# Performance work log

Hardware: AMD Instinct MI355X
Metric: run time of the kernel (lower is better)

## Reference

```python
import jax, jax.numpy as jnp
import numpy as np

B, T, C = 1, 2048, 2048
H, KV, D = 16, 4, 128
PAST = 2048


def setup_inputs() -> dict:
    key = jax.random.key(0)
    ks = jax.random.split(key, 11)
    return {
        "x": jax.random.normal(ks[0], (B, T, C), jnp.float32),
        "ve": jax.random.normal(ks[1], (B, T, KV * D), jnp.float32),
        "cos": jax.random.normal(ks[2], (1, T, 1, D // 2), jnp.float32),
        "sin": jax.random.normal(ks[3], (1, T, 1, D // 2), jnp.float32),
        "past_key": jax.random.normal(ks[4], (B, PAST, KV, D), jnp.float32),
        "past_value": jax.random.normal(ks[5], (B, PAST, KV, D), jnp.float32),
        "Wq": jax.random.normal(ks[6], (C, H * D), jnp.float32) * 0.02,
        "Wk": jax.random.normal(ks[7], (C, KV * D), jnp.float32) * 0.02,
        "Wv": jax.random.normal(ks[8], (C, KV * D), jnp.float32) * 0.02,
        "Wo": jax.random.normal(ks[9], (H * D, C), jnp.float32) * 0.02,
        "Wg": jax.random.normal(ks[10], (12, KV), jnp.float32),
    }


def _rmsnorm(x):
    return x * jax.lax.rsqrt(jnp.mean(x * x, axis=-1, keepdims=True) + 1e-6)


def _rope(x, cos, sin):
    # x: (B,T,heads,D); cos/sin: (1,T,1,D//2) broadcast over heads
    d = x.shape[-1] // 2
    x1, x2 = x[..., :d], x[..., d:]
    return jnp.concatenate([x1 * cos + x2 * sin, -x1 * sin + x2 * cos], axis=-1)


def reference(x, ve, cos, sin, past_key, past_value, Wq, Wk, Wv, Wo, Wg):
    Bx, Tx, Cx = x.shape
    G = H // KV
    q = (x @ Wq).reshape(Bx, Tx, H, D)
    k = (x @ Wk).reshape(Bx, Tx, KV, D)
    v = (x @ Wv).reshape(Bx, Tx, KV, D)
    # value-embedding gate: 3*sigmoid over first 12 channels of x
    gate = 3.0 * jax.nn.sigmoid(x[..., :12] @ Wg)  # (B,T,KV)
    v = v + gate[..., None] * ve.reshape(Bx, Tx, KV, D)
    q = _rmsnorm(_rope(q, cos, sin)) * 1.2
    k = _rmsnorm(_rope(k, cos, sin)) * 1.2
    present_key = jnp.concatenate([past_key, k], axis=1)    # (B,S,KV,D)
    present_value = jnp.concatenate([past_value, v], axis=1)
    S = present_key.shape[1]
    q_t = q.transpose(0, 2, 1, 3)                           # (B,H,T,D)
    k_t = present_key.transpose(0, 2, 1, 3)                 # (B,KV,S,D)
    v_t = present_value.transpose(0, 2, 1, 3)
    # GQA expansion: repeat each kv head G times -> (B,H,S,D)
    k_t = jnp.broadcast_to(k_t[:, :, None], (Bx, KV, G, S, D)).reshape(Bx, H, S, D)
    v_t = jnp.broadcast_to(v_t[:, :, None], (Bx, KV, G, S, D)).reshape(Bx, H, S, D)
    scale = D ** -0.5
    scores = jnp.einsum("bhtd,bhsd->bhts", q_t, k_t) * scale
    query_pos = jnp.arange(S - Tx, S)[:, None]
    key_pos = jnp.arange(S)[None, :]
    causal = key_pos <= query_pos                           # (T,S)
    scores = jnp.where(causal[None, None], scores, -jnp.inf)
    w = jax.nn.softmax(scores, axis=-1)
    y = jnp.einsum("bhts,bhsd->bthd", w, v_t).reshape(Bx, Tx, H * D)
    y = y @ Wo
    return (y, present_key, present_value)
```

## Files before the change

kernel.cpp:

```cpp
#include <hip/hip_runtime.h>
#include <hip/hip_bf16.h>
#include <math.h>

typedef __attribute__((ext_vector_type(8))) short short8;
typedef __attribute__((ext_vector_type(4))) short short4v;
typedef __attribute__((ext_vector_type(4))) float f32x4;

#define DEV __device__ __forceinline__

DEV short f2bf(float f) {
  unsigned u = __builtin_bit_cast(unsigned, f);
  unsigned r = (u + 0x7FFFu + ((u >> 16) & 1u)) >> 16;
  return (short)r;
}

DEV float bf2f(short s) {
  unsigned u = ((unsigned)(unsigned short)s) << 16;
  return __builtin_bit_cast(float, u);
}

DEV short f2h(float f) {
  _Float16 h = (_Float16)f;
  return __builtin_bit_cast(short, h);
}

DEV float h2f(short s) {
  return (float)__builtin_bit_cast(_Float16, s);
}

DEV unsigned cvt_pk_bf16(float lo, float hi) {
  unsigned r;
  asm("v_cvt_pk_bf16_f32 %0, %1, %2" : "=v"(r) : "v"(lo), "v"(hi));
  return r;
}

DEV void gload_lds16(const void* g, void* l) {
  __builtin_amdgcn_global_load_lds((const __attribute__((address_space(1))) void*)g,
                                   (__attribute__((address_space(3))) void*)l, 16, 0, 0);
}

__global__ __launch_bounds__(256) void gemm_m64_f32(const short* __restrict__ A,
                                                    const short* __restrict__ BT,
                                                    float* __restrict__ C,
                                                    int M, int N, int K) {
  __shared__ __attribute__((aligned(16))) short As[2][64 * 64];
  __shared__ __attribute__((aligned(16))) short Bs[2][128 * 64];
  const int tid = threadIdx.x;
  const int w = tid >> 6, l = tid & 63;
  const int g = l >> 4, lr = l & 15;
  int nbx = gridDim.x, nwg = nbx * gridDim.y;
  int flat = blockIdx.y * nbx + blockIdx.x;
  int qq = nwg >> 3;
  int f2 = (flat & 7) * qq + (flat >> 3);
  const int m0 = (f2 / nbx) * 64, n0 = (f2 % nbx) * 128;
  const int wr = w >> 1, wc = w & 1;
  f32x4 acc[2][4] = {};

  auto stage = [&](int buf, int k0) {
#pragma unroll
    for (int it = 0; it < 2; ++it) {
      int idx = it * 256 + tid;
      int row = idx >> 3;
      int scol = ((idx & 7) * 16) ^ ((row & 7) << 4);
      gload_lds16(A + (size_t)(m0 + row) * K + k0 + (scol >> 1), As[buf] + idx * 8);
    }
#pragma unroll
    for (int it = 0; it < 4; ++it) {
      int idx = it * 256 + tid;
      int row = idx >> 3;
      int scol = ((idx & 7) * 16) ^ ((row & 7) << 4);
      gload_lds16(BT + (size_t)(n0 + row) * K + k0 + (scol >> 1), Bs[buf] + idx * 8);
    }
  };

  stage(0, 0);
  __syncthreads();
  int cur = 0;
  for (int k0 = 0; k0 < K; k0 += 64) {
    if (k0 + 64 < K) stage(cur ^ 1, k0 + 64);
#pragma unroll
    for (int ki = 0; ki < 2; ++ki) {
      const int kcol = (ki * 64 + g * 16) ^ ((lr & 7) << 4);
      short8 af[2], bfr[4];
#pragma unroll
      for (int i = 0; i < 2; ++i)
        af[i] = *(const short8*)(As[cur] + (((wr * 32 + i * 16 + lr) * 128 + kcol) >> 1));
#pragma unroll
      for (int i = 0; i < 4; ++i)
        bfr[i] = *(const short8*)(Bs[cur] + (((wc * 64 + i * 16 + lr) * 128 + kcol) >> 1));
#pragma unroll
      for (int mi = 0; mi < 2; ++mi)
#pragma unroll
        for (int ni = 0; ni < 4; ++ni)
          acc[mi][ni] = __builtin_amdgcn_mfma_f32_16x16x32_bf16(af[mi], bfr[ni], acc[mi][ni], 0, 0, 0);
    }
    __syncthreads();
    cur ^= 1;
  }
#pragma unroll
  for (int mi = 0; mi < 2; ++mi)
#pragma unroll
    for (int ni = 0; ni < 4; ++ni) {
      int row = m0 + wr * 32 + mi * 16 + g * 4;
      int col = n0 + wc * 64 + ni * 16 + lr;
#pragma unroll
      for (int r = 0; r < 4; ++r)
        C[(size_t)(row + r) * N + col] = acc[mi][ni][r];
    }
}

__global__ __launch_bounds__(256) void gemm_m64_bf16(const short* __restrict__ A,
                                                     const short* __restrict__ BT,
                                                     short* __restrict__ C,
                                                     int M, int N, int K) {
  __shared__ __attribute__((aligned(16))) short As[2][64 * 64];
  __shared__ __attribute__((aligned(16))) short Bs[2][128 * 64];
  const int tid = threadIdx.x;
  const int w = tid >> 6, l = tid & 63;
  const int g = l >> 4, lr = l & 15;
  int nbx = gridDim.x, nwg = nbx * gridDim.y;
  int flat = blockIdx.y * nbx + blockIdx.x;
  int qq = nwg >> 3;
  int f2 = (flat & 7) * qq + (flat >> 3);
  const int m0 = (f2 / nbx) * 64, n0 = (f2 % nbx) * 128;
  const int wr = w >> 1, wc = w & 1;
  f32x4 acc[2][4] = {};

  auto stage = [&](int buf, int k0) {
#pragma unroll
    for (int it = 0; it < 2; ++it) {
      int idx = it * 256 + tid;
      int row = idx >> 3;
      int scol = ((idx & 7) * 16) ^ ((row & 7) << 4);
      gload_lds16(A + (size_t)(m0 + row) * K + k0 + (scol >> 1), As[buf] + idx * 8);
    }
#pragma unroll
    for (int it = 0; it < 4; ++it) {
      int idx = it * 256 + tid;
      int row = idx >> 3;
      int scol = ((idx & 7) * 16) ^ ((row & 7) << 4);
      gload_lds16(BT + (size_t)(n0 + row) * K + k0 + (scol >> 1), Bs[buf] + idx * 8);
    }
  };

  stage(0, 0);
  __syncthreads();
  int cur = 0;
  for (int k0 = 0; k0 < K; k0 += 64) {
    if (k0 + 64 < K) stage(cur ^ 1, k0 + 64);
#pragma unroll
    for (int ki = 0; ki < 2; ++ki) {
      const int kcol = (ki * 64 + g * 16) ^ ((lr & 7) << 4);
      short8 af[2], bfr[4];
#pragma unroll
      for (int i = 0; i < 2; ++i)
        af[i] = *(const short8*)(As[cur] + (((wr * 32 + i * 16 + lr) * 128 + kcol) >> 1));
#pragma unroll
      for (int i = 0; i < 4; ++i)
        bfr[i] = *(const short8*)(Bs[cur] + (((wc * 64 + i * 16 + lr) * 128 + kcol) >> 1));
#pragma unroll
      for (int mi = 0; mi < 2; ++mi)
#pragma unroll
        for (int ni = 0; ni < 4; ++ni)
          acc[mi][ni] = __builtin_amdgcn_mfma_f32_16x16x32_bf16(af[mi], bfr[ni], acc[mi][ni], 0, 0, 0);
    }
    __syncthreads();
    cur ^= 1;
  }
#pragma unroll
  for (int mi = 0; mi < 2; ++mi)
#pragma unroll
    for (int ni = 0; ni < 4; ++ni) {
      int row = m0 + wr * 32 + mi * 16 + g * 4;
      int col = n0 + wc * 64 + ni * 16 + lr;
#pragma unroll
      for (int r = 0; r < 4; ++r)
        C[(size_t)(row + r) * N + col] = f2bf(acc[mi][ni][r]);
    }
}

__global__ __launch_bounds__(256) void prep(const float* __restrict__ x,
                                            short* __restrict__ xb,
                                            const float* __restrict__ Wq,
                                            const float* __restrict__ Wk,
                                            const float* __restrict__ Wv,
                                            const float* __restrict__ Wo,
                                            short* __restrict__ WTqkv,
                                            short* __restrict__ WToT) {
  __shared__ float tile[32][33];
  int bid = blockIdx.x;
  int tid = threadIdx.x;
  if (bid < 4096) {
    int i = bid * 256 + tid;
    float4 v = ((const float4*)x)[i];
    short4v o;
    o.x = f2bf(v.x); o.y = f2bf(v.y); o.z = f2bf(v.z); o.w = f2bf(v.w);
    ((short4v*)xb)[i] = o;
    return;
  }
  int b = bid - 4096;
  int bx = b % 160, by = b / 160;
  const float* W;
  short* WT;
  int N, cb;
  if (bx < 64) { W = Wq; WT = WTqkv; N = 2048; cb = bx; }
  else if (bx < 80) { W = Wk; WT = WTqkv + (size_t)2048 * 2048; N = 512; cb = bx - 64; }
  else if (bx < 96) { W = Wv; WT = WTqkv + (size_t)2560 * 2048; N = 512; cb = bx - 80; }
  else { W = Wo; WT = WToT; N = 2048; cb = bx - 96; }
  int tx = tid & 31, ty = tid >> 5;
  int c0 = cb * 32, r0 = by * 32;
#pragma unroll
  for (int i = 0; i < 4; ++i)
    tile[ty + i * 8][tx] = W[(size_t)(r0 + ty + i * 8) * N + c0 + tx];
  __syncthreads();
#pragma unroll
  for (int i = 0; i < 4; ++i)
    WT[(size_t)(c0 + ty + i * 8) * 2048 + r0 + tx] = f2bf(tile[tx][ty + i * 8]);
}

__global__ __launch_bounds__(256) void qkv_post(const short* __restrict__ qkv,
                                                const float* __restrict__ cosb,
                                                const float* __restrict__ sinb,
                                                const float* __restrict__ x,
                                                const float* __restrict__ ve,
                                                const float* __restrict__ Wg,
                                                float* __restrict__ outPK,
                                                float* __restrict__ outPV,
                                                short* __restrict__ qb,
                                                short* __restrict__ kb) {
  int gw = (blockIdx.x * 256 + threadIdx.x) >> 6;
  int l = threadIdx.x & 63;
  int t = gw / 24, u = gw - t * 24;
  if (t >= 2048) return;
  if (u < 20) {
    float c = cosb[t * 64 + l], s = sinb[t * 64 + l];
    const short* src = qkv + (size_t)t * 3072 + (u < 16 ? u * 128 : 2048 + (u - 16) * 128);
    float x1 = bf2f(src[l]), x2 = bf2f(src[64 + l]);
    float lo = x1 * c + x2 * s;
    float hi = x2 * c - x1 * s;
    float ss = lo * lo + hi * hi;
#pragma unroll
    for (int d = 1; d < 64; d <<= 1) ss += __shfl_xor(ss, d, 64);
    float r = rsqrtf(ss * (1.0f / 128.0f) + 1e-6f) * 1.2f;
    if (u < 16) {
      const float SCQ = 0.08838834764831845f * 1.4426950408889634f;
      float rq = r * SCQ;
      size_t b = ((size_t)u * 2048 + t) * 128;
      qb[b + l] = f2bf(lo * rq);
      qb[b + 64 + l] = f2bf(hi * rq);
    } else {
      lo *= r; hi *= r;
      int kvh = u - 16;
      size_t b = ((size_t)(2048 + t) * 4 + kvh) * 128;
      outPK[b + l] = lo;
      outPK[b + 64 + l] = hi;
      size_t b2 = ((size_t)kvh * 4096 + 2048 + t) * 128;
      kb[b2 + l] = f2bf(lo);
      kb[b2 + 64 + l] = f2bf(hi);
    }
  } else {
    int kv = u - 20;
    float z = 0.f;
#pragma unroll
    for (int j = 0; j < 12; ++j) z += x[(size_t)t * 2048 + j] * Wg[j * 4 + kv];
    float gate = 3.0f / (1.0f + expf(-z));
    const short* vr = qkv + (size_t)t * 3072 + 2560 + kv * 128;
    const float* vei = ve + (size_t)t * 512 + kv * 128;
    float v0 = bf2f(vr[l]) + gate * vei[l];
    float v1 = bf2f(vr[64 + l]) + gate * vei[64 + l];
    size_t b = ((size_t)(2048 + t) * 4 + kv) * 128;
    outPV[b + l] = v0;
    outPV[b + 64 + l] = v1;
  }
}

__global__ __launch_bounds__(256) void past_copy(const float* __restrict__ pk,
                                                 float* __restrict__ outPK,
                                                 short* __restrict__ kb) {
  int i = blockIdx.x * 256 + threadIdx.x;
  int d = i & 127, kv = (i >> 7) & 3, s = i >> 9;
  float a = pk[i];
  outPK[i] = a;
  kb[((size_t)kv * 4096 + s) * 128 + d] = f2bf(a);
}

__global__ __launch_bounds__(256) void v_transpose(const float* __restrict__ pv,
                                                   float* __restrict__ outPV,
                                                   short* __restrict__ vbT) {
  __shared__ float tile[32][33];
  int tx = threadIdx.x & 31, ty = threadIdx.x >> 5;
  int c0 = blockIdx.x * 32, r0 = blockIdx.y * 32;
  if (r0 < 2048) {
#pragma unroll
    for (int i = 0; i < 4; ++i) {
      float v = pv[(size_t)(r0 + ty + i * 8) * 512 + c0 + tx];
      tile[ty + i * 8][tx] = v;
      outPV[(size_t)(r0 + ty + i * 8) * 512 + c0 + tx] = v;
    }
  } else {
#pragma unroll
    for (int i = 0; i < 4; ++i)
      tile[ty + i * 8][tx] = outPV[(size_t)(r0 + ty + i * 8) * 512 + c0 + tx];
  }
  __syncthreads();
#pragma unroll
  for (int i = 0; i < 4; ++i)
    vbT[(size_t)(c0 + ty + i * 8) * 4096 + r0 + tx] = f2bf(tile[tx][ty + i * 8]);
}

__global__ __launch_bounds__(256, 2) void attn(const short* __restrict__ qb,
                                               const short* __restrict__ kb,
                                               const short* __restrict__ vbT,
                                               short* __restrict__ Po,
                                               float* __restrict__ ml) {
  extern __shared__ __attribute__((aligned(16))) short smem[];
  short* Ks = smem;
  short* Vs = smem + 16384;
  const int tid = threadIdx.x, w = tid >> 6, l = tid & 63;
  const int g = l >> 4, lr = l & 15;
  const int lid = blockIdx.x;
  const int qbi = 15 - (lid >> 5);
  const int sub = lid & 31;
  const int h = sub >> 1, cls = sub & 1;
  const int kv = h >> 2;
  const int qw = qbi * 128 + w * 32;
  char* Pw = (char*)(smem + 32768) + w * 2048;
  const short* gK = kb + (size_t)kv * 4096 * 128;
  const short* gV = vbT + (size_t)kv * 128 * 4096;
  const int nT = 34 + 2 * qbi;
  const int cnt = (nT - cls + 1) >> 1;

  short8 aq[2][4];
#pragma unroll
  for (int u = 0; u < 2; ++u)
#pragma unroll
    for (int c4 = 0; c4 < 4; ++c4)
      aq[u][c4] = *(const short8*)(qb + ((size_t)(h * 2048 + qw + u * 16 + lr)) * 128 + c4 * 32 + g * 8);

  float m_r[2] = {-INFINITY, -INFINITY};
  float l_r[2] = {0.f, 0.f};
  f32x4 o[2][8] = {};

  const int rK = tid >> 4, cKs = ((tid & 15) * 16) ^ ((rK & 7) << 4);
  const int rV = tid >> 3, cVs = ((tid & 7) * 16) ^ ((rV & 7) << 4);
  const short* kptr = gK + (size_t)(cls * 64 + rK) * 128 + (cKs >> 1);
  const short* vptr = gV + (size_t)rV * 4096 + cls * 64 + (cVs >> 1);
  short* kdst = Ks + w * 512;
  short* vdst = Vs + w * 512;

  auto stageK = [&](int buf) {
#pragma unroll
    for (int it = 0; it < 4; ++it)
      gload_lds16(kptr + it * 2048, kdst + buf * 8192 + it * 2048);
    kptr += 16384;
  };
  auto stageV = [&](int buf) {
#pragma unroll
    for (int it = 0; it < 4; ++it)
      gload_lds16(vptr + (size_t)it * 131072, vdst + buf * 8192 + it * 2048);
    vptr += 128;
  };

  stageK(0);
  stageV(0);
  __syncthreads();
  int cur = 0;
  for (int i = 0; i < cnt; ++i) {
    const int s0 = (cls + 2 * i) * 64;
    if (i + 1 < cnt) {
      stageK(cur ^ 1);
      stageV(cur ^ 1);
    }
    f32x4 sc[2][4] = {};
    __builtin_amdgcn_s_setprio(1);
#pragma unroll
    for (int cc = 0; cc < 4; ++cc) {
      const int rb = cur * 8192 + (cc * 16 + lr) * 128;
      short8 bk[4];
#pragma unroll
      for (int c4 = 0; c4 < 4; ++c4)
        bk[c4] = *(const short8*)(Ks + rb + (((c4 * 64 + g * 16) ^ ((lr & 7) << 4)) >> 1));
#pragma unroll
      for (int c4 = 0; c4 < 4; ++c4) {
        sc[0][cc] = __builtin_amdgcn_mfma_f32_16x16x32_bf16(bk[c4], aq[0][c4], sc[0][cc], 0, 0, 0);
        sc[1][cc] = __builtin_amdgcn_mfma_f32_16x16x32_bf16(bk[c4], aq[1][c4], sc[1][cc], 0, 0, 0);
      }
    }
    __builtin_amdgcn_s_setprio(0);
    if (s0 + 63 > 2048 + qw) {
#pragma unroll
      for (int u = 0; u < 2; ++u)
#pragma unroll
        for (int cc = 0; cc < 4; ++cc)
#pragma unroll
          for (int r = 0; r < 4; ++r)
            sc[u][cc][r] = (s0 + cc * 16 + g * 4 + r <= 2048 + qw + u * 16 + lr)
                               ? sc[u][cc][r] : -INFINITY;
    }
    short8 ap[2][2];
#pragma unroll
    for (int u = 0; u < 2; ++u) {
      float pmax = -INFINITY;
#pragma unroll
      for (int cc = 0; cc < 4; ++cc) {
        float a = fmaxf(fmaxf(sc[u][cc][0], sc[u][cc][1]), fmaxf(sc[u][cc][2], sc[u][cc][3]));
        pmax = fmaxf(pmax, a);
      }
      if (!__all(pmax - m_r[u] <= 8.0f)) {
        float tm = fmaxf(pmax, __shfl_xor(pmax, 16, 64));
        tm = fmaxf(tm, __shfl_xor(tm, 32, 64));
        float mn = fmaxf(m_r[u], tm);
        float corr = exp2f(m_r[u] - mn);
        m_r[u] = mn;
        l_r[u] *= corr;
        float co[4];
#pragma unroll
        for (int r = 0; r < 4; ++r) co[r] = __shfl(corr, (l & 48) | (g * 4 + r), 64);
#pragma unroll
        for (int d8 = 0; d8 < 8; ++d8) {
          f32x4 tt = o[u][d8];
#pragma unroll
          for (int r = 0; r < 4; ++r) tt[r] *= co[r];
          o[u][d8] = tt;
        }
      }
      float ps = 0.f;
#pragma unroll
      for (int cc = 0; cc < 4; ++cc) {
        float p0 = exp2f(sc[u][cc][0] - m_r[u]);
        float p1 = exp2f(sc[u][cc][1] - m_r[u]);
        float p2 = exp2f(sc[u][cc][2] - m_r[u]);
        float p3 = exp2f(sc[u][cc][3] - m_r[u]);
        ps += (p0 + p1) + (p2 + p3);
        unsigned pk0 = cvt_pk_bf16(p0, p1);
        unsigned pk1 = cvt_pk_bf16(p2, p3);
        int off8 = (lr * 128 + cc * 32 + g * 8) ^ ((lr & 7) << 4);
        unsigned long long pq = (unsigned long long)pk0 | ((unsigned long long)pk1 << 32);
        *(unsigned long long*)(Pw + off8) = pq;
      }
      l_r[u] += ps;
#pragma unroll
      for (int ks = 0; ks < 2; ++ks)
        ap[u][ks] = *(const short8*)(Pw + ((lr * 128 + ks * 64 + g * 16) ^ ((lr & 7) << 4)));
    }
    __builtin_amdgcn_s_setprio(1);
#pragma unroll
    for (int d8 = 0; d8 < 8; ++d8) {
      const int rb = cur * 8192 + (d8 * 16 + lr) * 64;
      short8 bv0 = *(const short8*)(Vs + rb + (((0 * 64 + g * 16) ^ ((lr & 7) << 4)) >> 1));
      short8 bv1 = *(const short8*)(Vs + rb + (((1 * 64 + g * 16) ^ ((lr & 7) << 4)) >> 1));
      o[0][d8] = __builtin_amdgcn_mfma_f32_16x16x32_bf16(ap[0][0], bv0, o[0][d8], 0, 0, 0);
      o[0][d8] = __builtin_amdgcn_mfma_f32_16x16x32_bf16(ap[0][1], bv1, o[0][d8], 0, 0, 0);
      o[1][d8] = __builtin_amdgcn_mfma_f32_16x16x32_bf16(ap[1][0], bv0, o[1][d8], 0, 0, 0);
      o[1][d8] = __builtin_amdgcn_mfma_f32_16x16x32_bf16(ap[1][1], bv1, o[1][d8], 0, 0, 0);
    }
    __builtin_amdgcn_s_setprio(0);
    __syncthreads();
    cur ^= 1;
  }
#pragma unroll
  for (int u = 0; u < 2; ++u) {
    float ls = l_r[u];
    ls += __shfl_xor(ls, 16, 64);
    ls += __shfl_xor(ls, 32, 64);
    float inv = 1.0f / ls;
    float invo[4];
#pragma unroll
    for (int r = 0; r < 4; ++r) invo[r] = __shfl(inv, (l & 48) | (g * 4 + r), 64);
#pragma unroll
    for (int d8 = 0; d8 < 8; ++d8)
#pragma unroll
      for (int r = 0; r < 4; ++r)
        Po[((size_t)(cls * 16 + h) * 2048 + qw + u * 16 + g * 4 + r) * 128 + d8 * 16 + lr] =
            f2h(o[u][d8][r] * invo[r]);
    if (g == 0) {
      float2 v;
      v.x = m_r[u];
      v.y = ls;
      ((float2*)ml)[(size_t)(cls * 16 + h) * 2048 + qw + u * 16 + lr] = v;
    }
  }
}

__global__ __launch_bounds__(256) void attn_merge(const short* __restrict__ Po,
                                                  const float* __restrict__ ml,
                                                  short* __restrict__ ya) {
  int i = blockIdx.x * 256 + threadIdx.x;
  int q = i >> 8, rem = i & 255, h = rem >> 4, oct = rem & 15;
  float mc[2], lc[2];
#pragma unroll
  for (int c = 0; c < 2; ++c) {
    float2 v = ((const float2*)ml)[(size_t)(c * 16 + h) * 2048 + q];
    mc[c] = v.x; lc[c] = v.y;
  }
  float m = fmaxf(mc[0], mc[1]);
  float wsum = 0.f, acc[8] = {};
#pragma unroll
  for (int c = 0; c < 2; ++c) {
    float wc = lc[c] * exp2f(mc[c] - m);
    wsum += wc;
    short8 p = *(const short8*)(Po + ((size_t)(c * 16 + h) * 2048 + q) * 128 + oct * 8);
#pragma unroll
    for (int j = 0; j < 8; ++j) acc[j] += wc * h2f(p[j]);
  }
  float inv = 1.0f / wsum;
  short8 ov;
#pragma unroll
  for (int j = 0; j < 8; ++j) ov[j] = f2bf(acc[j] * inv);
  *(short8*)(ya + (size_t)q * 2048 + h * 128 + oct * 8) = ov;
}

extern "C" void kernel_launch(void* const* d_in, const int* in_sizes, int n_in,
                              void* d_out, int out_size, void* d_ws, size_t ws_size,
                              hipStream_t stream) {
  const float* x = (const float*)d_in[0];
  const float* ve = (const float*)d_in[1];
  const float* cosb = (const float*)d_in[2];
  const float* sinb = (const float*)d_in[3];
  const float* past_key = (const float*)d_in[4];
  const float* past_value = (const float*)d_in[5];
  const float* Wq = (const float*)d_in[6];
  const float* Wk = (const float*)d_in[7];
  const float* Wv = (const float*)d_in[8];
  const float* Wo = (const float*)d_in[9];
  const float* Wg = (const float*)d_in[10];

  float* outY = (float*)d_out;
  float* outPK = outY + 4194304;
  float* outPV = outPK + 2097152;

  short* base = (short*)d_ws;
  short* WToT = base;
  short* WTqkv = base + 4194304;
  short* xb = WTqkv + (size_t)6291456;
  short* qkv = xb + (size_t)4194304;
  short* qb = qkv + (size_t)12582912;
  short* kb = qb + (size_t)4194304;
  short* vbT = kb + (size_t)2097152;
  short* ya = vbT + (size_t)2097152;
  short* Po = WTqkv;
  float* mlb = (float*)(base + 20971520);

  static bool attr_set = false;
  if (!attr_set) {
    (void)hipFuncSetAttribute((const void*)attn,
                              hipFuncAttributeMaxDynamicSharedMemorySize, 73728);
    attr_set = true;
  }

  prep<<<14336, 256, 0, stream>>>(x, xb, Wq, Wk, Wv, Wo, WTqkv, WToT);

  gemm_m64_bf16<<<dim3(24, 32), 256, 0, stream>>>(xb, WTqkv, qkv, 2048, 3072, 2048);

  qkv_post<<<12288, 256, 0, stream>>>(qkv, cosb, sinb, x, ve, Wg, outPK, outPV, qb, kb);
  past_copy<<<4096, 256, 0, stream>>>(past_key, outPK, kb);
  v_transpose<<<dim3(16, 128), 256, 0, stream>>>(past_value, outPV, vbT);

  attn<<<512, 256, 73728, stream>>>(qb, kb, vbT, Po, mlb);
  attn_merge<<<2048, 256, 0, stream>>>(Po, mlb, ya);

  gemm_m64_f32<<<dim3(16, 32), 256, 0, stream>>>(ya, WToT, outY, 2048, 2048, 2048);
}
```

Baseline: 181.0 us.

## Fuse RoPE, RMSNorm and value gating into the QKV GEMM epilogue

The QKV projection GEMM now stages its fp32 accumulator tile in shared memory and applies RoPE, RMSNorm, the Q scaling and the value-embedding gate directly in the epilogue. This removes the separate qkv_post kernel and the bf16 round trip of the qkv intermediate through global memory. Because no bf16 rounding happens before normalization, precision improves slightly. In exchange the GEMM epilogue gets longer, and shared memory grows to 48KB to hold the 64x132 fp32 tile, which could lower occupancy.

```diff
diff --git a/kernel.cpp b/kernel.cpp
--- a/kernel.cpp
+++ b/kernel.cpp
@@ -37,6 +37,132 @@
 DEV void gload_lds16(const void* g, void* l) {
   __builtin_amdgcn_global_load_lds((const __attribute__((address_space(1))) void*)g,
                                    (__attribute__((address_space(3))) void*)l, 16, 0, 0);
+}
+
+__global__ __launch_bounds__(256) void gemm_qkv_fused(const short* __restrict__ A,
+                                                      const short* __restrict__ BT,
+                                                      const float* __restrict__ cosb,
+                                                      const float* __restrict__ sinb,
+                                                      const float* __restrict__ x,
+                                                      const float* __restrict__ ve,
+                                                      const float* __restrict__ Wg,
+                                                      float* __restrict__ outPK,
+                                                      float* __restrict__ outPV,
+                                                      short* __restrict__ qb,
+                                                      short* __restrict__ kb) {
+  const int K = 2048;
+  __shared__ __attribute__((aligned(16))) char smem[49152];
+  short* As0 = (short*)smem;
+  short* Bs0 = (short*)(smem + 16384);
+  const int tid = threadIdx.x;
+  const int w = tid >> 6, l = tid & 63;
+  const int g = l >> 4, lr = l & 15;
+  int nbx = gridDim.x, nwg = nbx * gridDim.y;
+  int flat = blockIdx.y * nbx + blockIdx.x;
+  int qq = nwg >> 3;
+  int f2 = (flat & 7) * qq + (flat >> 3);
+  const int m0 = (f2 / nbx) * 64;
+  const int j = f2 % nbx;
+  const int n0 = j * 128;
+  const int wr = w >> 1, wc = w & 1;
+  f32x4 acc[2][4] = {};
+
+  auto stage = [&](int buf, int k0) {
+#pragma unroll
+    for (int it = 0; it < 2; ++it) {
+      int idx = it * 256 + tid;
+      int row = idx >> 3;
+      int scol = ((idx & 7) * 16) ^ ((row & 7) << 4);
+      gload_lds16(A + (size_t)(m0 + row) * K + k0 + (scol >> 1), As0 + buf * 4096 + idx * 8);
+    }
+#pragma unroll
+    for (int it = 0; it < 4; ++it) {
+      int idx = it * 256 + tid;
+      int row = idx >> 3;
+      int scol = ((idx & 7) * 16) ^ ((row & 7) << 4);
+      gload_lds16(BT + (size_t)(n0 + row) * K + k0 + (scol >> 1), Bs0 + buf * 8192 + idx * 8);
+    }
+  };
+
+  stage(0, 0);
+  __syncthreads();
+  int cur = 0;
+  for (int k0 = 0; k0 < K; k0 += 64) {
+    if (k0 + 64 < K) stage(cur ^ 1, k0 + 64);
+#pragma unroll
+    for (int ki = 0; ki < 2; ++ki) {
+      const int kcol = (ki * 64 + g * 16) ^ ((lr & 7) << 4);
+      short8 af[2], bfr[4];
+#pragma unroll
+      for (int i = 0; i < 2; ++i)
+        af[i] = *(const short8*)(As0 + cur * 4096 + (((wr * 32 + i * 16 + lr) * 128 + kcol) >> 1));
+#pragma unroll
+      for (int i = 0; i < 4; ++i)
+        bfr[i] = *(const short8*)(Bs0 + cur * 8192 + (((wc * 64 + i * 16 + lr) * 128 + kcol) >> 1));
+#pragma unroll
+      for (int mi = 0; mi < 2; ++mi)
+#pragma unroll
+        for (int ni = 0; ni < 4; ++ni)
+          acc[mi][ni] = __builtin_amdgcn_mfma_f32_16x16x32_bf16(af[mi], bfr[ni], acc[mi][ni], 0, 0, 0);
+    }
+    __syncthreads();
+    cur ^= 1;
+  }
+  float* tile = (float*)smem;
+#pragma unroll
+  for (int mi = 0; mi < 2; ++mi)
+#pragma unroll
+    for (int ni = 0; ni < 4; ++ni) {
+      int rrow = wr * 32 + mi * 16 + g * 4;
+      int col = wc * 64 + ni * 16 + lr;
+#pragma unroll
+      for (int r = 0; r < 4; ++r)
+        tile[(rrow + r) * 132 + col] = acc[mi][ni][r];
+    }
+  __syncthreads();
+  const float SCQ = 0.08838834764831845f * 1.4426950408889634f;
+  for (int rr = 0; rr < 16; ++rr) {
+    int tl = w * 16 + rr;
+    int t = m0 + tl;
+    float x1 = tile[tl * 132 + l];
+    float x2 = tile[tl * 132 + 64 + l];
+    if (j < 20) {
+      float c = cosb[t * 64 + l], s = sinb[t * 64 + l];
+      float lo = x1 * c + x2 * s;
+      float hi = x2 * c - x1 * s;
+      float ss = lo * lo + hi * hi;
+#pragma unroll
+      for (int d = 1; d < 64; d <<= 1) ss += __shfl_xor(ss, d, 64);
+      float r = rsqrtf(ss * (1.0f / 128.0f) + 1e-6f) * 1.2f;
+      if (j < 16) {
+        float rq = r * SCQ;
+        size_t b = ((size_t)j * 2048 + t) * 128;
+        qb[b + l] = f2bf(lo * rq);
+        qb[b + 64 + l] = f2bf(hi * rq);
+      } else {
+        lo *= r; hi *= r;
+        int kvh = j - 16;
+        size_t b = ((size_t)(2048 + t) * 4 + kvh) * 128;
+        outPK[b + l] = lo;
+        outPK[b + 64 + l] = hi;
+        size_t b2 = ((size_t)kvh * 4096 + 2048 + t) * 128;
+        kb[b2 + l] = f2bf(lo);
+        kb[b2 + 64 + l] = f2bf(hi);
+      }
+    } else {
+      int kv = j - 20;
+      float z = 0.f;
+#pragma unroll
+      for (int jj = 0; jj < 12; ++jj) z += x[(size_t)t * 2048 + jj] * Wg[jj * 4 + kv];
+      float gate = 3.0f / (1.0f + expf(-z));
+      const float* vei = ve + (size_t)t * 512 + kv * 128;
+      float v0 = x1 + gate * vei[l];
+      float v1 = x2 + gate * vei[64 + l];
+      size_t b = ((size_t)(2048 + t) * 4 + kv) * 128;
+      outPV[b + l] = v0;
+      outPV[b + 64 + l] = v1;
+    }
+  }
 }
 
 __global__ __launch_bounds__(256) void gemm_m64_f32(const short* __restrict__ A,
@@ -106,76 +232,6 @@
 #pragma unroll
       for (int r = 0; r < 4; ++r)
         C[(size_t)(row + r) * N + col] = acc[mi][ni][r];
-    }
-}
-
-__global__ __launch_bounds__(256) void gemm_m64_bf16(const short* __restrict__ A,
-                                                     const short* __restrict__ BT,
-                                                     short* __restrict__ C,
-                                                     int M, int N, int K) {
-  __shared__ __attribute__((aligned(16))) short As[2][64 * 64];
-  __shared__ __attribute__((aligned(16))) short Bs[2][128 * 64];
-  const int tid = threadIdx.x;
-  const int w = tid >> 6, l = tid & 63;
-  const int g = l >> 4, lr = l & 15;
-  int nbx = gridDim.x, nwg = nbx * gridDim.y;
-  int flat = blockIdx.y * nbx + blockIdx.x;
-  int qq = nwg >> 3;
-  int f2 = (flat & 7) * qq + (flat >> 3);
-  const int m0 = (f2 / nbx) * 64, n0 = (f2 % nbx) * 128;
-  const int wr = w >> 1, wc = w & 1;
-  f32x4 acc[2][4] = {};
-
-  auto stage = [&](int buf, int k0) {
-#pragma unroll
-    for (int it = 0; it < 2; ++it) {
-      int idx = it * 256 + tid;
-      int row = idx >> 3;
-      int scol = ((idx & 7) * 16) ^ ((row & 7) << 4);
-      gload_lds16(A + (size_t)(m0 + row) * K + k0 + (scol >> 1), As[buf] + idx * 8);
-    }
-#pragma unroll
-    for (int it = 0; it < 4; ++it) {
-      int idx = it * 256 + tid;
-      int row = idx >> 3;
-      int scol = ((idx & 7) * 16) ^ ((row & 7) << 4);
-      gload_lds16(BT + (size_t)(n0 + row) * K + k0 + (scol >> 1), Bs[buf] + idx * 8);
-    }
-  };
-
-  stage(0, 0);
-  __syncthreads();
-  int cur = 0;
-  for (int k0 = 0; k0 < K; k0 += 64) {
-    if (k0 + 64 < K) stage(cur ^ 1, k0 + 64);
-#pragma unroll
-    for (int ki = 0; ki < 2; ++ki) {
-      const int kcol = (ki * 64 + g * 16) ^ ((lr & 7) << 4);
-      short8 af[2], bfr[4];
-#pragma unroll
-      for (int i = 0; i < 2; ++i)
-        af[i] = *(const short8*)(As[cur] + (((wr * 32 + i * 16 + lr) * 128 + kcol) >> 1));
-#pragma unroll
-      for (int i = 0; i < 4; ++i)
-        bfr[i] = *(const short8*)(Bs[cur] + (((wc * 64 + i * 16 + lr) * 128 + kcol) >> 1));
-#pragma unroll
-      for (int mi = 0; mi < 2; ++mi)
-#pragma unroll
-        for (int ni = 0; ni < 4; ++ni)
-          acc[mi][ni] = __builtin_amdgcn_mfma_f32_16x16x32_bf16(af[mi], bfr[ni], acc[mi][ni], 0, 0, 0);
-    }
-    __syncthreads();
-    cur ^= 1;
-  }
-#pragma unroll
-  for (int mi = 0; mi < 2; ++mi)
-#pragma unroll
-    for (int ni = 0; ni < 4; ++ni) {
-      int row = m0 + wr * 32 + mi * 16 + g * 4;
-      int col = n0 + wc * 64 + ni * 16 + lr;
-#pragma unroll
-      for (int r = 0; r < 4; ++r)
-        C[(size_t)(row + r) * N + col] = f2bf(acc[mi][ni][r]);
     }
 }
 
@@ -216,62 +272,6 @@
 #pragma unroll
   for (int i = 0; i < 4; ++i)
     WT[(size_t)(c0 + ty + i * 8) * 2048 + r0 + tx] = f2bf(tile[tx][ty + i * 8]);
-}
-
-__global__ __launch_bounds__(256) void qkv_post(const short* __restrict__ qkv,
-                                                const float* __restrict__ cosb,
-                                                const float* __restrict__ sinb,
-                                                const float* __restrict__ x,
-                                                const float* __restrict__ ve,
-                                                const float* __restrict__ Wg,
-                                                float* __restrict__ outPK,
-                                                float* __restrict__ outPV,
-                                                short* __restrict__ qb,
-                                                short* __restrict__ kb) {
-  int gw = (blockIdx.x * 256 + threadIdx.x) >> 6;
-  int l = threadIdx.x & 63;
-  int t = gw / 24, u = gw - t * 24;
-  if (t >= 2048) return;
-  if (u < 20) {
-    float c = cosb[t * 64 + l], s = sinb[t * 64 + l];
-    const short* src = qkv + (size_t)t * 3072 + (u < 16 ? u * 128 : 2048 + (u - 16) * 128);
-    float x1 = bf2f(src[l]), x2 = bf2f(src[64 + l]);
-    float lo = x1 * c + x2 * s;
-    float hi = x2 * c - x1 * s;
-    float ss = lo * lo + hi * hi;
-#pragma unroll
-    for (int d = 1; d < 64; d <<= 1) ss += __shfl_xor(ss, d, 64);
-    float r = rsqrtf(ss * (1.0f / 128.0f) + 1e-6f) * 1.2f;
-    if (u < 16) {
-      const float SCQ = 0.08838834764831845f * 1.4426950408889634f;
-      float rq = r * SCQ;
-      size_t b = ((size_t)u * 2048 + t) * 128;
-      qb[b + l] = f2bf(lo * rq);
-      qb[b + 64 + l] = f2bf(hi * rq);
-    } else {
-      lo *= r; hi *= r;
-      int kvh = u - 16;
-      size_t b = ((size_t)(2048 + t) * 4 + kvh) * 128;
-      outPK[b + l] = lo;
-      outPK[b + 64 + l] = hi;
-      size_t b2 = ((size_t)kvh * 4096 + 2048 + t) * 128;
-      kb[b2 + l] = f2bf(lo);
-      kb[b2 + 64 + l] = f2bf(hi);
-    }
-  } else {
-    int kv = u - 20;
-    float z = 0.f;
-#pragma unroll
-    for (int j = 0; j < 12; ++j) z += x[(size_t)t * 2048 + j] * Wg[j * 4 + kv];
-    float gate = 3.0f / (1.0f + expf(-z));
-    const short* vr = qkv + (size_t)t * 3072 + 2560 + kv * 128;
-    const float* vei = ve + (size_t)t * 512 + kv * 128;
-    float v0 = bf2f(vr[l]) + gate * vei[l];
-    float v1 = bf2f(vr[64 + l]) + gate * vei[64 + l];
-    size_t b = ((size_t)(2048 + t) * 4 + kv) * 128;
-    outPV[b + l] = v0;
-    outPV[b + 64 + l] = v1;
-  }
 }
 
 __global__ __launch_bounds__(256) void past_copy(const float* __restrict__ pk,
@@ -533,8 +533,7 @@
   short* WToT = base;
   short* WTqkv = base + 4194304;
   short* xb = WTqkv + (size_t)6291456;
-  short* qkv = xb + (size_t)4194304;
-  short* qb = qkv + (size_t)12582912;
+  short* qb = xb + (size_t)4194304 + 12582912;
   short* kb = qb + (size_t)4194304;
   short* vbT = kb + (size_t)2097152;
   short* ya = vbT + (size_t)2097152;
@@ -550,9 +549,9 @@
 
   prep<<<14336, 256, 0, stream>>>(x, xb, Wq, Wk, Wv, Wo, WTqkv, WToT);
 
-  gemm_m64_bf16<<<dim3(24, 32), 256, 0, stream>>>(xb, WTqkv, qkv, 2048, 3072, 2048);
-
-  qkv_post<<<12288, 256, 0, stream>>>(qkv, cosb, sinb, x, ve, Wg, outPK, outPV, qb, kb);
+  gemm_qkv_fused<<<dim3(24, 32), 256, 0, stream>>>(xb, WTqkv, cosb, sinb, x, ve, Wg,
+                                                   outPK, outPV, qb, kb);
+
   past_copy<<<4096, 256, 0, stream>>>(past_key, outPK, kb);
   v_transpose<<<dim3(16, 128), 256, 0, stream>>>(past_value, outPV, vbT);
 
```

Result: no change. 182.8 us (+1.0%).
